# Optimization experiments

Hardware: AMD Instinct MI355X
Metric: run time of the kernel (lower is better)

Reference implementation:

```python
import jax, jax.numpy as jnp
import numpy as np

BS, NQ, NC, NT = 16, 900, 91, 1600
COST_CLASS, COST_BBOX, COST_GIOU = 1.0, 5.0, 2.0


def box_cxcywh_to_xyxy(b):
    cx, cy, w, h = b[..., 0], b[..., 1], b[..., 2], b[..., 3]
    return jnp.stack([cx - 0.5 * w, cy - 0.5 * h, cx + 0.5 * w, cy + 0.5 * h], axis=-1)


def generalized_box_iou(boxes1, boxes2):
    # boxes1: [N,4] xyxy, boxes2: [M,4] xyxy -> [N,M]
    area1 = (boxes1[:, 2] - boxes1[:, 0]) * (boxes1[:, 3] - boxes1[:, 1])  # [N]
    area2 = (boxes2[:, 2] - boxes2[:, 0]) * (boxes2[:, 3] - boxes2[:, 1])  # [M]
    lt = jnp.maximum(boxes1[:, None, :2], boxes2[None, :, :2])  # [N,M,2]
    rb = jnp.minimum(boxes1[:, None, 2:], boxes2[None, :, 2:])  # [N,M,2]
    wh = jnp.clip(rb - lt, 0.0)
    inter = wh[..., 0] * wh[..., 1]  # [N,M]
    union = area1[:, None] + area2[None, :] - inter
    iou = inter / union
    # smallest enclosing box
    lt_c = jnp.minimum(boxes1[:, None, :2], boxes2[None, :, :2])
    rb_c = jnp.maximum(boxes1[:, None, 2:], boxes2[None, :, 2:])
    wh_c = jnp.clip(rb_c - lt_c, 0.0)
    area_c = wh_c[..., 0] * wh_c[..., 1]
    return iou - (area_c - union) / area_c


def setup_inputs() -> dict:
    key = jax.random.key(0)
    k1, k2, k3, k4 = jax.random.split(key, 4)
    pred_logits = jax.random.normal(k1, (BS, NQ, NC), dtype=jnp.float32)
    # cxcywh in (0,1): guarantee positive w,h and sane boxes
    pred_boxes = jax.random.uniform(k2, (BS, NQ, 4), dtype=jnp.float32, minval=0.05, maxval=0.95)
    tgt_bbox = jax.random.uniform(k3, (NT, 4), dtype=jnp.float32, minval=0.05, maxval=0.95)
    tgt_ids = jax.random.randint(k4, (NT,), 0, NC, dtype=jnp.int32)
    return {"pred_logits": pred_logits, "pred_boxes": pred_boxes,
            "tgt_bbox": tgt_bbox, "tgt_ids": tgt_ids}


def reference(pred_logits, pred_boxes, tgt_bbox, tgt_ids):
    bs, num_queries = pred_logits.shape[:2]
    out_prob = jax.nn.softmax(pred_logits.reshape(-1, pred_logits.shape[-1]), axis=-1)  # [bs*nq, NC]
    out_bbox = pred_boxes.reshape(-1, 4)  # [bs*nq, 4]
    cost_class = -out_prob[:, tgt_ids]  # [bs*nq, NT]
    # L1 cdist
    cost_bbox = jnp.sum(jnp.abs(out_bbox[:, None, :] - tgt_bbox[None, :, :]), axis=-1)
    cost_giou = -generalized_box_iou(box_cxcywh_to_xyxy(out_bbox), box_cxcywh_to_xyxy(tgt_bbox))
    C = COST_BBOX * cost_bbox + COST_CLASS * cost_class + COST_GIOU * cost_giou
    return C.reshape(bs, num_queries, -1)
```

## Files before the change

### kernel.cpp

```cpp
#include <hip/hip_runtime.h>
#include <math.h>

#define BS_ 16
#define NQ_ 900
#define NC_ 91
#define NT_ 1600
#define NROWS_ (BS_ * NQ_)
#define TILE_R 4
#define TPB 320
#define NBLK (NROWS_ / TILE_R)
#define KITER (NT_ / TPB)

__global__ __launch_bounds__(TPB) void matcher_cost_kernel(
    const float* __restrict__ logits,
    const float* __restrict__ pboxes,
    const float4* __restrict__ tboxes,
    const int*   __restrict__ tids,
    float* __restrict__ out)
{
    const int base = blockIdx.x * TILE_R;
    const int tid  = threadIdx.x;
    const int lane = tid & 63;
    const int wave = tid >> 6;

    __shared__ __align__(16) float sneg[NC_ * TILE_R];

    if (wave < TILE_R) {
        const float* lrow = logits + (base + wave) * NC_;
        float v0 = lrow[lane];
        float v1 = (lane < NC_ - 64) ? lrow[64 + lane] : -INFINITY;
        float m = fmaxf(v0, v1);
        #pragma unroll
        for (int off = 32; off >= 1; off >>= 1)
            m = fmaxf(m, __shfl_xor(m, off, 64));
        float e0 = __expf(v0 - m);
        float e1 = (lane < NC_ - 64) ? __expf(v1 - m) : 0.0f;
        float s = e0 + e1;
        #pragma unroll
        for (int off = 32; off >= 1; off >>= 1)
            s += __shfl_xor(s, off, 64);
        const float inv_s = __builtin_amdgcn_rcpf(s);
        sneg[lane * TILE_R + wave] = fmaf(-e0, inv_s, 2.0f);
        if (lane < NC_ - 64)
            sneg[(64 + lane) * TILE_R + wave] = fmaf(-e1, inv_s, 2.0f);
    }

    float4 tb[KITER];
    int    id[KITER];
    #pragma unroll
    for (int k = 0; k < KITER; ++k) {
        const int j = k * TPB + tid;
        tb[k] = tboxes[j];
        id[k] = tids[j];
    }

    float qcx[TILE_R], qcy[TILE_R], qw[TILE_R], qh[TILE_R];
    float qx0[TILE_R], qy0[TILE_R], qx1[TILE_R], qy1[TILE_R], qarea[TILE_R];
    #pragma unroll
    for (int r = 0; r < TILE_R; ++r) {
        const float4 qb = *reinterpret_cast<const float4*>(pboxes + (base + r) * 4);
        qcx[r] = qb.x; qcy[r] = qb.y; qw[r] = qb.z; qh[r] = qb.w;
        qx0[r] = fmaf(-0.5f, qb.z, qb.x);
        qy0[r] = fmaf(-0.5f, qb.w, qb.y);
        qx1[r] = fmaf( 0.5f, qb.z, qb.x);
        qy1[r] = fmaf( 0.5f, qb.w, qb.y);
        qarea[r] = qb.z * qb.w;
    }

    __syncthreads();

    float4 pp[KITER];
    #pragma unroll
    for (int k = 0; k < KITER; ++k)
        pp[k] = *reinterpret_cast<const float4*>(&sneg[id[k] * TILE_R]);

    #pragma unroll
    for (int k = 0; k < KITER; ++k) {
        const int j = k * TPB + tid;
        const float4 t = tb[k];
        const float tx0 = fmaf(-0.5f, t.z, t.x);
        const float ty0 = fmaf(-0.5f, t.w, t.y);
        const float tx1 = fmaf( 0.5f, t.z, t.x);
        const float ty1 = fmaf( 0.5f, t.w, t.y);
        const float tarea = t.z * t.w;
        const float p[TILE_R] = {pp[k].x, pp[k].y, pp[k].z, pp[k].w};

        #pragma unroll
        for (int r = 0; r < TILE_R; ++r) {
            const float cb = fabsf(qcx[r] - t.x) + fabsf(qcy[r] - t.y)
                           + fabsf(qw[r]  - t.z) + fabsf(qh[r]  - t.w);

            const float dx = fminf(qx1[r], tx1) - fmaxf(qx0[r], tx0);
            const float dy = fminf(qy1[r], ty1) - fmaxf(qy0[r], ty0);
            const float inter = fmaxf(dx, 0.0f) * fmaxf(dy, 0.0f);
            const float uni   = (qarea[r] + tarea) - inter;

            const float cw = (qw[r] + t.z) - dx;
            const float ch = (qh[r] + t.w) - dy;
            const float areac = cw * ch;

            float c = fmaf(5.0f, cb, p[r]);
            c = fmaf(-2.0f * inter, __builtin_amdgcn_rcpf(uni),   c);
            c = fmaf(-2.0f * uni,   __builtin_amdgcn_rcpf(areac), c);

            __builtin_nontemporal_store(c, out + (base + r) * NT_ + j);
        }
    }
}

extern "C" void kernel_launch(void* const* d_in, const int* in_sizes, int n_in,
                              void* d_out, int out_size, void* d_ws, size_t ws_size,
                              hipStream_t stream) {
    const float*  logits = (const float*)d_in[0];
    const float*  pboxes = (const float*)d_in[1];
    const float4* tboxes = (const float4*)d_in[2];
    const int*    tids   = (const int*)d_in[3];
    float* out = (float*)d_out;

    matcher_cost_kernel<<<NBLK, TPB, 0, stream>>>(logits, pboxes, tboxes, tids, out);
}
```

Measured before the change: 119.1 us.

## Split into row-table precompute kernel and vectorized 128-bit-store sweep kernel

Adds a first kernel that computes per-row softmax class costs and query box corner tables into workspace, and a second sweep kernel in which each thread emits four consecutive target costs as a single 128-bit nontemporal store. The sweep gathers class probabilities from a global row table instead of LDS. The aim is wider, more efficient output writes and removal of the in-block softmax and barrier. In exchange it adds a second launch, a workspace round trip, and scattered global gathers. It falls back to the original fused kernel when the workspace is too small.

```diff
diff --git a/kernel.cpp b/kernel.cpp
--- a/kernel.cpp
+++ b/kernel.cpp
@@ -10,6 +10,126 @@
 #define TPB 320
 #define NBLK (NROWS_ / TILE_R)
 #define KITER (NT_ / TPB)
+#define GITER 5
+#define PT_LD 96
+#define QT_LD 12
+#define PT_FLOATS (NROWS_ * PT_LD)
+#define QT_FLOATS (NROWS_ * QT_LD)
+
+typedef float f32x4 __attribute__((ext_vector_type(4)));
+
+__global__ __launch_bounds__(256) void row_tables_kernel(
+    const float* __restrict__ logits,
+    const float* __restrict__ pboxes,
+    float* __restrict__ pt,
+    float* __restrict__ qt)
+{
+    const int wave = threadIdx.x >> 6;
+    const int lane = threadIdx.x & 63;
+    const int row  = blockIdx.x * 4 + wave;
+
+    const float* lrow = logits + row * NC_;
+    float v0 = lrow[lane];
+    float v1 = (lane < NC_ - 64) ? lrow[64 + lane] : -INFINITY;
+    float m = fmaxf(v0, v1);
+    #pragma unroll
+    for (int off = 32; off >= 1; off >>= 1)
+        m = fmaxf(m, __shfl_xor(m, off, 64));
+    float e0 = __expf(v0 - m);
+    float e1 = (lane < NC_ - 64) ? __expf(v1 - m) : 0.0f;
+    float s = e0 + e1;
+    #pragma unroll
+    for (int off = 32; off >= 1; off >>= 1)
+        s += __shfl_xor(s, off, 64);
+    const float inv_s = __builtin_amdgcn_rcpf(s);
+    pt[row * PT_LD + lane] = fmaf(-e0, inv_s, 2.0f);
+    if (lane < NC_ - 64)
+        pt[row * PT_LD + 64 + lane] = fmaf(-e1, inv_s, 2.0f);
+
+    if (lane == 0) {
+        const float4 qb = reinterpret_cast<const float4*>(pboxes)[row];
+        float4 a;
+        a.x = qb.x; a.y = qb.y; a.z = qb.z; a.w = qb.w;
+        float4 b;
+        b.x = fmaf(-0.5f, qb.z, qb.x);
+        b.y = fmaf(-0.5f, qb.w, qb.y);
+        b.z = fmaf( 0.5f, qb.z, qb.x);
+        b.w = fmaf( 0.5f, qb.w, qb.y);
+        float4* q4 = reinterpret_cast<float4*>(qt + row * QT_LD);
+        q4[0] = a;
+        q4[1] = b;
+        qt[row * QT_LD + 8] = qb.z * qb.w;
+    }
+}
+
+__device__ __forceinline__ float cost_one(const float4 q0, const float4 q1,
+                                          const float qarea, const float4 t,
+                                          const float p)
+{
+    const float cb = fabsf(q0.x - t.x) + fabsf(q0.y - t.y)
+                   + fabsf(q0.z - t.z) + fabsf(q0.w - t.w);
+    const float tx0 = fmaf(-0.5f, t.z, t.x);
+    const float ty0 = fmaf(-0.5f, t.w, t.y);
+    const float tx1 = fmaf( 0.5f, t.z, t.x);
+    const float ty1 = fmaf( 0.5f, t.w, t.y);
+    const float tarea = t.z * t.w;
+    const float dx = fminf(q1.z, tx1) - fmaxf(q1.x, tx0);
+    const float dy = fminf(q1.w, ty1) - fmaxf(q1.y, ty0);
+    const float inter = fmaxf(dx, 0.0f) * fmaxf(dy, 0.0f);
+    const float uni   = (qarea + tarea) - inter;
+    const float cw = (q0.z + t.z) - dx;
+    const float ch = (q0.w + t.w) - dy;
+    const float areac = cw * ch;
+    float c = fmaf(5.0f, cb, p);
+    c = fmaf(-2.0f * inter, __builtin_amdgcn_rcpf(uni),   c);
+    c = fmaf(-2.0f * uni,   __builtin_amdgcn_rcpf(areac), c);
+    return c;
+}
+
+__global__ __launch_bounds__(TPB) void sweep_kernel(
+    const float*  __restrict__ pt,
+    const float*  __restrict__ qt,
+    const float4* __restrict__ tboxes,
+    const int4*   __restrict__ tids4,
+    f32x4*        __restrict__ out4)
+{
+    const unsigned base = blockIdx.x * TILE_R;
+    const unsigned tid  = threadIdx.x;
+    f32x4* outp = out4 + base * (NT_ / 4) + tid;
+
+    #pragma unroll 1
+    for (int k = 0; k < GITER; ++k) {
+        const unsigned g    = (unsigned)k * TPB + tid;
+        const unsigned row  = g / 400u;
+        const unsigned jb   = g - row * 400u;
+        const unsigned grow = base + row;
+
+        const int4   id = tids4[jb];
+        const float4 tA = tboxes[4u * jb + 0u];
+        const float4 tB = tboxes[4u * jb + 1u];
+        const float4 tC = tboxes[4u * jb + 2u];
+        const float4 tD = tboxes[4u * jb + 3u];
+
+        const float* qrow = qt + grow * QT_LD;
+        const float4 q0 = *reinterpret_cast<const float4*>(qrow);
+        const float4 q1 = *reinterpret_cast<const float4*>(qrow + 4);
+        const float  qarea = qrow[8];
+
+        const float* prow = pt + grow * PT_LD;
+        const float pA = prow[id.x];
+        const float pB = prow[id.y];
+        const float pC = prow[id.z];
+        const float pD = prow[id.w];
+
+        f32x4 c;
+        c.x = cost_one(q0, q1, qarea, tA, pA);
+        c.y = cost_one(q0, q1, qarea, tB, pB);
+        c.z = cost_one(q0, q1, qarea, tC, pC);
+        c.w = cost_one(q0, q1, qarea, tD, pD);
+
+        __builtin_nontemporal_store(c, outp + k * TPB);
+    }
+}
 
 __global__ __launch_bounds__(TPB) void matcher_cost_kernel(
     const float* __restrict__ logits,
@@ -89,20 +209,16 @@
         for (int r = 0; r < TILE_R; ++r) {
             const float cb = fabsf(qcx[r] - t.x) + fabsf(qcy[r] - t.y)
                            + fabsf(qw[r]  - t.z) + fabsf(qh[r]  - t.w);
-
             const float dx = fminf(qx1[r], tx1) - fmaxf(qx0[r], tx0);
             const float dy = fminf(qy1[r], ty1) - fmaxf(qy0[r], ty0);
             const float inter = fmaxf(dx, 0.0f) * fmaxf(dy, 0.0f);
             const float uni   = (qarea[r] + tarea) - inter;
-
             const float cw = (qw[r] + t.z) - dx;
             const float ch = (qh[r] + t.w) - dy;
             const float areac = cw * ch;
-
             float c = fmaf(5.0f, cb, p[r]);
             c = fmaf(-2.0f * inter, __builtin_amdgcn_rcpf(uni),   c);
             c = fmaf(-2.0f * uni,   __builtin_amdgcn_rcpf(areac), c);
-
             __builtin_nontemporal_store(c, out + (base + r) * NT_ + j);
         }
     }
@@ -117,5 +233,14 @@
     const int*    tids   = (const int*)d_in[3];
     float* out = (float*)d_out;
 
-    matcher_cost_kernel<<<NBLK, TPB, 0, stream>>>(logits, pboxes, tboxes, tids, out);
-}
+    const size_t need = (size_t)(PT_FLOATS + QT_FLOATS) * sizeof(float);
+    if (d_ws != nullptr && ws_size >= need) {
+        float* pt = (float*)d_ws;
+        float* qt = pt + PT_FLOATS;
+        row_tables_kernel<<<NROWS_ / 4, 256, 0, stream>>>(logits, (const float*)d_in[1], pt, qt);
+        sweep_kernel<<<NBLK, TPB, 0, stream>>>(pt, qt, tboxes,
+                                               (const int4*)tids, (f32x4*)out);
+    } else {
+        matcher_cost_kernel<<<NBLK, TPB, 0, stream>>>(logits, pboxes, tboxes, tids, out);
+    }
+}
```

Result: slower. 146.2 us (+22.8%).

## Split softmax into precompute kernel and merge GIoU reciprocals into one

Applied to the files above, without the earlier changes.

Adds a separate kernel that computes per-row softmax probabilities (without max subtraction) into a workspace table laid out per block. The main sweep kernel then copies that table into LDS instead of computing softmax itself, so the softmax no longer sits at the start of every output block. The two reciprocals in the GIoU term are combined into a single reciprocal of uni*areac, which saves one transcendental per element. The cost is an extra launch, a workspace round trip, and possible overflow in expf because the max is no longer subtracted.

```diff
diff --git a/kernel.cpp b/kernel.cpp
--- a/kernel.cpp
+++ b/kernel.cpp
@@ -10,6 +10,107 @@
 #define TPB 320
 #define NBLK (NROWS_ / TILE_R)
 #define KITER (NT_ / TPB)
+#define PT_BLK 384
+#define PT_FLOATS (NBLK * PT_BLK)
+
+__global__ __launch_bounds__(256) void softmax_table_kernel(
+    const float* __restrict__ logits,
+    float* __restrict__ pt)
+{
+    const int w    = threadIdx.x >> 6;
+    const int lane = threadIdx.x & 63;
+    const int row  = blockIdx.x * TILE_R + w;
+
+    const float* lrow = logits + row * NC_;
+    const float e0 = __expf(lrow[lane]);
+    const float e1 = (lane < NC_ - 64) ? __expf(lrow[64 + lane]) : 0.0f;
+    float s = e0 + e1;
+    #pragma unroll
+    for (int off = 32; off >= 1; off >>= 1)
+        s += __shfl_xor(s, off, 64);
+    const float inv_s = __builtin_amdgcn_rcpf(s);
+
+    float* dst = pt + blockIdx.x * PT_BLK + w;
+    dst[lane * 4] = fmaf(-e0, inv_s, 2.0f);
+    if (lane < NC_ - 64)
+        dst[(64 + lane) * 4] = fmaf(-e1, inv_s, 2.0f);
+}
+
+__global__ __launch_bounds__(TPB) void sweep_lds_kernel(
+    const float* __restrict__ pt,
+    const float* __restrict__ pboxes,
+    const float4* __restrict__ tboxes,
+    const int*   __restrict__ tids,
+    float* __restrict__ out)
+{
+    const int base = blockIdx.x * TILE_R;
+    const int tid  = threadIdx.x;
+
+    __shared__ __align__(16) float sneg[PT_BLK];
+
+    if (tid < PT_BLK / 4)
+        reinterpret_cast<float4*>(sneg)[tid] =
+            reinterpret_cast<const float4*>(pt + blockIdx.x * PT_BLK)[tid];
+
+    float4 tb[KITER];
+    int    id[KITER];
+    #pragma unroll
+    for (int k = 0; k < KITER; ++k) {
+        const int j = k * TPB + tid;
+        tb[k] = tboxes[j];
+        id[k] = tids[j];
+    }
+
+    float qcx[TILE_R], qcy[TILE_R], qw[TILE_R], qh[TILE_R];
+    float qx0[TILE_R], qy0[TILE_R], qx1[TILE_R], qy1[TILE_R], qarea[TILE_R];
+    #pragma unroll
+    for (int r = 0; r < TILE_R; ++r) {
+        const float4 qb = *reinterpret_cast<const float4*>(pboxes + (base + r) * 4);
+        qcx[r] = qb.x; qcy[r] = qb.y; qw[r] = qb.z; qh[r] = qb.w;
+        qx0[r] = fmaf(-0.5f, qb.z, qb.x);
+        qy0[r] = fmaf(-0.5f, qb.w, qb.y);
+        qx1[r] = fmaf( 0.5f, qb.z, qb.x);
+        qy1[r] = fmaf( 0.5f, qb.w, qb.y);
+        qarea[r] = qb.z * qb.w;
+    }
+
+    __syncthreads();
+
+    float4 pp[KITER];
+    #pragma unroll
+    for (int k = 0; k < KITER; ++k)
+        pp[k] = *reinterpret_cast<const float4*>(&sneg[id[k] * 4]);
+
+    #pragma unroll
+    for (int k = 0; k < KITER; ++k) {
+        const int j = k * TPB + tid;
+        const float4 t = tb[k];
+        const float tx0 = fmaf(-0.5f, t.z, t.x);
+        const float ty0 = fmaf(-0.5f, t.w, t.y);
+        const float tx1 = fmaf( 0.5f, t.z, t.x);
+        const float ty1 = fmaf( 0.5f, t.w, t.y);
+        const float tarea = t.z * t.w;
+        const float p[TILE_R] = {pp[k].x, pp[k].y, pp[k].z, pp[k].w};
+
+        #pragma unroll
+        for (int r = 0; r < TILE_R; ++r) {
+            const float cb = fabsf(qcx[r] - t.x) + fabsf(qcy[r] - t.y)
+                           + fabsf(qw[r]  - t.z) + fabsf(qh[r]  - t.w);
+            const float dx = fminf(qx1[r], tx1) - fmaxf(qx0[r], tx0);
+            const float dy = fminf(qy1[r], ty1) - fmaxf(qy0[r], ty0);
+            const float inter = fmaxf(dx, 0.0f) * fmaxf(dy, 0.0f);
+            const float uni   = (qarea[r] + tarea) - inter;
+            const float cw = (qw[r] + t.z) - dx;
+            const float ch = (qh[r] + t.w) - dy;
+            const float areac = cw * ch;
+            const float num = fmaf(uni, uni, inter * areac);
+            const float den = uni * areac;
+            float c = fmaf(5.0f, cb, p[r]);
+            c = fmaf(-2.0f * num, __builtin_amdgcn_rcpf(den), c);
+            __builtin_nontemporal_store(c, out + (base + r) * NT_ + j);
+        }
+    }
+}
 
 __global__ __launch_bounds__(TPB) void matcher_cost_kernel(
     const float* __restrict__ logits,
@@ -89,20 +190,16 @@
         for (int r = 0; r < TILE_R; ++r) {
             const float cb = fabsf(qcx[r] - t.x) + fabsf(qcy[r] - t.y)
                            + fabsf(qw[r]  - t.z) + fabsf(qh[r]  - t.w);
-
             const float dx = fminf(qx1[r], tx1) - fmaxf(qx0[r], tx0);
             const float dy = fminf(qy1[r], ty1) - fmaxf(qy0[r], ty0);
             const float inter = fmaxf(dx, 0.0f) * fmaxf(dy, 0.0f);
             const float uni   = (qarea[r] + tarea) - inter;
-
             const float cw = (qw[r] + t.z) - dx;
             const float ch = (qh[r] + t.w) - dy;
             const float areac = cw * ch;
-
             float c = fmaf(5.0f, cb, p[r]);
             c = fmaf(-2.0f * inter, __builtin_amdgcn_rcpf(uni),   c);
             c = fmaf(-2.0f * uni,   __builtin_amdgcn_rcpf(areac), c);
-
             __builtin_nontemporal_store(c, out + (base + r) * NT_ + j);
         }
     }
@@ -117,5 +214,12 @@
     const int*    tids   = (const int*)d_in[3];
     float* out = (float*)d_out;
 
-    matcher_cost_kernel<<<NBLK, TPB, 0, stream>>>(logits, pboxes, tboxes, tids, out);
-}
+    const size_t need = (size_t)PT_FLOATS * sizeof(float);
+    if (d_ws != nullptr && ws_size >= need) {
+        float* pt = (float*)d_ws;
+        softmax_table_kernel<<<NBLK, 256, 0, stream>>>(logits, pt);
+        sweep_lds_kernel<<<NBLK, TPB, 0, stream>>>(pt, pboxes, tboxes, tids, out);
+    } else {
+        matcher_cost_kernel<<<NBLK, TPB, 0, stream>>>(logits, pboxes, tboxes, tids, out);
+    }
+}
```

Measured after the change: 117.3 us. No clear change (-1.5%).

## Split into softmax table pre-pass and vectorized float4-store sweep kernel

Applied to the files above, without the earlier changes.

A first kernel computes the per-row class cost table into workspace, dropping the max subtraction from the softmax, and transposes the target boxes into structure-of-arrays form. A second kernel assigns each thread one query row and four consecutive targets, so it can issue 16-byte nontemporal stores, and it prefetches the next target group ahead of use. The GIoU term is folded into a single reciprocal, num/(uni*areac). This adds a second launch and a workspace round trip. Removing the max subtraction risks overflow for large logits, and the merged division may change rounding slightly.

```diff
diff --git a/kernel.cpp b/kernel.cpp
--- a/kernel.cpp
+++ b/kernel.cpp
@@ -10,6 +10,141 @@
 #define TPB 320
 #define NBLK (NROWS_ / TILE_R)
 #define KITER (NT_ / TPB)
+#define PT_LD 96
+#define PT_BLK (TILE_R * PT_LD)
+#define PT_FLOATS (NBLK * PT_BLK)
+#define SOA_FLOATS (4 * NT_)
+#define GPR 400
+#define GPT 80
+
+typedef float f32x4 __attribute__((ext_vector_type(4)));
+
+__global__ __launch_bounds__(256) void table_kernel(
+    const float*  __restrict__ logits,
+    const float4* __restrict__ tboxes,
+    float* __restrict__ pt,
+    float* __restrict__ soa)
+{
+    const int w    = threadIdx.x >> 6;
+    const int lane = threadIdx.x & 63;
+    const int row  = blockIdx.x * TILE_R + w;
+
+    const float* lrow = logits + row * NC_;
+    const float e0 = __expf(lrow[lane]);
+    const float e1 = (lane < NC_ - 64) ? __expf(lrow[64 + lane]) : 0.0f;
+    float s = e0 + e1;
+    #pragma unroll
+    for (int off = 32; off >= 1; off >>= 1)
+        s += __shfl_xor(s, off, 64);
+    const float inv_s = __builtin_amdgcn_rcpf(s);
+
+    float* dst = pt + row * PT_LD;
+    dst[lane] = fmaf(-e0, inv_s, 2.0f);
+    if (lane < NC_ - 64)
+        dst[64 + lane] = fmaf(-e1, inv_s, 2.0f);
+
+    if (blockIdx.x < 7) {
+        const int i = blockIdx.x * 256 + threadIdx.x;
+        if (i < NT_) {
+            const float4 t = tboxes[i];
+            soa[i]           = t.x;
+            soa[NT_ + i]     = t.y;
+            soa[2 * NT_ + i] = t.z;
+            soa[3 * NT_ + i] = t.w;
+        }
+    }
+}
+
+__device__ __forceinline__ float cost1(
+    float qcx, float qcy, float qw, float qh,
+    float qx0, float qy0, float qx1, float qy1, float qarea,
+    float tcx, float tcy, float tw, float th, float p)
+{
+    const float cb = fabsf(qcx - tcx) + fabsf(qcy - tcy)
+                   + fabsf(qw - tw)  + fabsf(qh - th);
+    const float tx0 = fmaf(-0.5f, tw, tcx);
+    const float ty0 = fmaf(-0.5f, th, tcy);
+    const float tx1 = fmaf( 0.5f, tw, tcx);
+    const float ty1 = fmaf( 0.5f, th, tcy);
+    const float dx = fminf(qx1, tx1) - fmaxf(qx0, tx0);
+    const float dy = fminf(qy1, ty1) - fmaxf(qy0, ty0);
+    const float inter = fmaxf(dx, 0.0f) * fmaxf(dy, 0.0f);
+    const float uni   = fmaf(tw, th, qarea) - inter;
+    const float cw = (qw + tw) - dx;
+    const float ch = (qh + th) - dy;
+    const float areac = cw * ch;
+    const float num = fmaf(uni, uni, inter * areac);
+    const float den = uni * areac;
+    const float c = fmaf(5.0f, cb, p);
+    return fmaf(-2.0f * num, __builtin_amdgcn_rcpf(den), c);
+}
+
+__global__ __launch_bounds__(TPB) void sweep_v4_kernel(
+    const float* __restrict__ pt,
+    const float* __restrict__ pboxes,
+    const float* __restrict__ soa,
+    const int*   __restrict__ tids,
+    f32x4*       __restrict__ out4)
+{
+    const int tid  = threadIdx.x;
+    const int blk  = blockIdx.x;
+    const int base = blk * TILE_R;
+    const int rt   = tid / GPT;
+    const int c0   = tid - rt * GPT;
+
+    __shared__ __align__(16) float sp[PT_BLK];
+
+    if (tid < PT_BLK / 4)
+        reinterpret_cast<f32x4*>(sp)[tid] =
+            reinterpret_cast<const f32x4*>(pt + blk * PT_BLK)[tid];
+
+    const float4 qb = *reinterpret_cast<const float4*>(pboxes + (base + rt) * 4);
+    const float qcx = qb.x, qcy = qb.y, qw = qb.z, qh = qb.w;
+    const float qx0 = fmaf(-0.5f, qb.z, qb.x);
+    const float qy0 = fmaf(-0.5f, qb.w, qb.y);
+    const float qx1 = fmaf( 0.5f, qb.z, qb.x);
+    const float qy1 = fmaf( 0.5f, qb.w, qb.y);
+    const float qarea = qb.z * qb.w;
+
+    const f32x4* txp = reinterpret_cast<const f32x4*>(soa);
+    const f32x4* typ = reinterpret_cast<const f32x4*>(soa + NT_);
+    const f32x4* twp = reinterpret_cast<const f32x4*>(soa + 2 * NT_);
+    const f32x4* thp = reinterpret_cast<const f32x4*>(soa + 3 * NT_);
+    const int4*  idp = reinterpret_cast<const int4*>(tids);
+
+    f32x4 tx = txp[c0], ty = typ[c0], tw = twp[c0], th = thp[c0];
+    int4  id = idp[c0];
+
+    const float* prow = sp + rt * PT_LD;
+    f32x4* outp = out4 + (base + rt) * GPR + c0;
+
+    __syncthreads();
+
+    #pragma unroll
+    for (int k = 0; k < 5; ++k) {
+        f32x4 ntx, nty, ntw, nth; int4 nid;
+        if (k < 4) {
+            const int jn = c0 + GPT * (k + 1);
+            ntx = txp[jn]; nty = typ[jn]; ntw = twp[jn]; nth = thp[jn];
+            nid = idp[jn];
+        }
+
+        const float pA = prow[id.x];
+        const float pB = prow[id.y];
+        const float pC = prow[id.z];
+        const float pD = prow[id.w];
+
+        f32x4 c;
+        c.x = cost1(qcx,qcy,qw,qh, qx0,qy0,qx1,qy1,qarea, tx.x,ty.x,tw.x,th.x, pA);
+        c.y = cost1(qcx,qcy,qw,qh, qx0,qy0,qx1,qy1,qarea, tx.y,ty.y,tw.y,th.y, pB);
+        c.z = cost1(qcx,qcy,qw,qh, qx0,qy0,qx1,qy1,qarea, tx.z,ty.z,tw.z,th.z, pC);
+        c.w = cost1(qcx,qcy,qw,qh, qx0,qy0,qx1,qy1,qarea, tx.w,ty.w,tw.w,th.w, pD);
+
+        __builtin_nontemporal_store(c, outp + GPT * k);
+
+        tx = ntx; ty = nty; tw = ntw; th = nth; id = nid;
+    }
+}
 
 __global__ __launch_bounds__(TPB) void matcher_cost_kernel(
     const float* __restrict__ logits,
@@ -89,20 +224,16 @@
         for (int r = 0; r < TILE_R; ++r) {
             const float cb = fabsf(qcx[r] - t.x) + fabsf(qcy[r] - t.y)
                            + fabsf(qw[r]  - t.z) + fabsf(qh[r]  - t.w);
-
             const float dx = fminf(qx1[r], tx1) - fmaxf(qx0[r], tx0);
             const float dy = fminf(qy1[r], ty1) - fmaxf(qy0[r], ty0);
             const float inter = fmaxf(dx, 0.0f) * fmaxf(dy, 0.0f);
             const float uni   = (qarea[r] + tarea) - inter;
-
             const float cw = (qw[r] + t.z) - dx;
             const float ch = (qh[r] + t.w) - dy;
             const float areac = cw * ch;
-
             float c = fmaf(5.0f, cb, p[r]);
             c = fmaf(-2.0f * inter, __builtin_amdgcn_rcpf(uni),   c);
             c = fmaf(-2.0f * uni,   __builtin_amdgcn_rcpf(areac), c);
-
             __builtin_nontemporal_store(c, out + (base + r) * NT_ + j);
         }
     }
@@ -117,5 +248,13 @@
     const int*    tids   = (const int*)d_in[3];
     float* out = (float*)d_out;
 
-    matcher_cost_kernel<<<NBLK, TPB, 0, stream>>>(logits, pboxes, tboxes, tids, out);
-}
+    const size_t need = (size_t)(PT_FLOATS + SOA_FLOATS) * sizeof(float);
+    if (d_ws != nullptr && ws_size >= need) {
+        float* pt  = (float*)d_ws;
+        float* soa = pt + PT_FLOATS;
+        table_kernel<<<NBLK, 256, 0, stream>>>(logits, tboxes, pt, soa);
+        sweep_v4_kernel<<<NBLK, TPB, 0, stream>>>(pt, pboxes, soa, tids, (f32x4*)out);
+    } else {
+        matcher_cost_kernel<<<NBLK, TPB, 0, stream>>>(logits, pboxes, tboxes, tids, out);
+    }
+}
```

Result: slower. 130.7 us (+9.7%).
